# Kernel tuning notes

Hardware: AMD Instinct MI355X
Metric: run time of the kernel (lower is better)

## Reference

```python
import jax, jax.numpy as jnp
import numpy as np

B, S, D, H, F = 2, 2048, 1024, 16, 4096
HD = D // H
EPS = 1e-5
NEG = -1e9


def _layernorm(x, g, b):
    mu = jnp.mean(x, axis=-1, keepdims=True)
    var = jnp.mean((x - mu) ** 2, axis=-1, keepdims=True)
    return (x - mu) * jax.lax.rsqrt(var + EPS) * g + b


def _attention(x, wq, wk, wv, wo, bo):
    b, s, d = x.shape
    q = (x @ wq).reshape(b, s, H, HD).transpose(0, 2, 1, 3)  # [b,h,s,hd]
    k = (x @ wk).reshape(b, s, H, HD).transpose(0, 2, 1, 3)
    v = (x @ wv).reshape(b, s, H, HD).transpose(0, 2, 1, 3)
    scores = jnp.einsum('bhqd,bhkd->bhqk', q, k) / (HD ** 0.5)
    # Faithful to source bug: masked_fill(mask == 0, -1e9) where mask = triu(diag=1)
    # -> positions with k <= q (lower triangle incl. diagonal) are filled with -1e9.
    lower = jnp.tril(jnp.ones((s, s), dtype=bool))
    scores = jnp.where(lower, NEG, scores)
    w = jax.nn.softmax(scores, axis=-1)
    o = jnp.einsum('bhqk,bhkd->bhqd', w, v)
    o = o.transpose(0, 2, 1, 3).reshape(b, s, d)
    return o @ wo + bo


def _ffn(x, w1, b1, w2, b2):
    return jax.nn.gelu(x @ w1 + b1, approximate=False) @ w2 + b2


def setup_inputs() -> dict:
    key = jax.random.key(0)
    ks = jax.random.split(key, 10)
    s = 0.02
    return {
        'x': jax.random.normal(ks[0], (B, S, D), jnp.float32),
        'wq': jax.random.normal(ks[1], (D, D), jnp.float32) * s,
        'wk': jax.random.normal(ks[2], (D, D), jnp.float32) * s,
        'wv': jax.random.normal(ks[3], (D, D), jnp.float32) * s,
        'wo': jax.random.normal(ks[4], (D, D), jnp.float32) * s,
        'bo': jnp.zeros((D,), jnp.float32),
        'ln1_g': jnp.ones((D,), jnp.float32),
        'ln1_b': jnp.zeros((D,), jnp.float32),
        'ln2_g': jnp.ones((D,), jnp.float32),
        'ln2_b': jnp.zeros((D,), jnp.float32),
        'w1': jax.random.normal(ks[5], (D, F), jnp.float32) * s,
        'b1': jnp.zeros((F,), jnp.float32),
        'w2': jax.random.normal(ks[6], (F, D), jnp.float32) * s,
        'b2': jnp.zeros((D,), jnp.float32),
    }


def reference(x, wq, wk, wv, wo, bo, ln1_g, ln1_b, ln2_g, ln2_b, w1, b1, w2, b2):
    shortcut = x
    h = _layernorm(x, ln1_g, ln1_b)
    h = _attention(h, wq, wk, wv, wo, bo)  # dropout = identity (eval)
    h = h + shortcut
    shortcut = h
    h2 = _layernorm(h, ln2_g, ln2_b)
    h2 = _attention(h2, wq, wk, wv, wo, bo)  # same attn module reused, per source
    h2 = _ffn(h2, w1, b1, w2, b2)
    return h2 + shortcut
```

## Files before the change

kernel.cpp:

```cpp
#include <hip/hip_runtime.h>
#include <hip/hip_bf16.h>
#include <math.h>

#define Bz 2
#define Sz 2048
#define Dz 1024
#define Hz 16
#define HDz 64
#define Fz 4096
#define ROWS (Bz*Sz)
#define EPSf 1e-5f
#define NEGf -1e9f

typedef __attribute__((ext_vector_type(8))) short short8;
typedef __attribute__((ext_vector_type(4))) float floatx4;

__device__ __forceinline__ unsigned short f2bf(float f){
  __hip_bfloat16 h = __float2bfloat16(f);
  return *(unsigned short*)&h;
}
__device__ __forceinline__ float bf2f(unsigned short u){
  union { unsigned x; float f; } a; a.x = ((unsigned)u) << 16; return a.f;
}

__device__ __forceinline__ float fast_gelu(float x){
  float t  = fabsf(x) * 0.70710678118654752f;
  float kk = __builtin_amdgcn_rcpf(1.0f + 0.3275911f * t);
  float poly = ((((1.061405429f*kk - 1.453152027f)*kk + 1.421413741f)*kk
                 - 0.284496736f)*kk + 0.254829592f)*kk;
  float er = 1.0f - poly * __expf(-t*t);
  er = copysignf(er, x);
  return 0.5f * x * (1.0f + er);
}

__device__ __forceinline__ void gload16(const void* g, void* l){
  __builtin_amdgcn_global_load_lds(
      (const __attribute__((address_space(1))) unsigned int*)g,
      (__attribute__((address_space(3))) unsigned int*)l, 16, 0, 0);
}

__device__ __forceinline__ void bar(){
  asm volatile("" ::: "memory");
  __builtin_amdgcn_s_barrier();
  asm volatile("" ::: "memory");
}
#define WAITV6 asm volatile("s_waitcnt vmcnt(6)" ::: "memory")
#define WAITV0 asm volatile("s_waitcnt vmcnt(0)" ::: "memory")
#define WL0    asm volatile("s_waitcnt lgkmcnt(0)" ::: "memory")

__device__ __forceinline__ void xcd_remap(int& bmblk, int& bnblk){
  int gx = gridDim.x, gy = gridDim.y;
  int id = blockIdx.y * gx + blockIdx.x;
  int xcd = id & 7, local = id >> 3;
  bnblk = local % gx;
  bmblk = xcd * (gy >> 3) + local / gx;
}

__global__ __launch_bounds__(256)
void transpose_cast(const float* __restrict__ W, unsigned short* __restrict__ Wt,
                    int K, int N)
{
  __shared__ unsigned short Ts[32][33];
  int n0 = blockIdx.x*32, k0 = blockIdx.y*32;
  int r = threadIdx.x >> 3, c0 = (threadIdx.x & 7) * 4;
  float4 w4 = *(const float4*)(W + (size_t)(k0+r)*N + n0 + c0);
  Ts[r][c0+0] = f2bf(w4.x); Ts[r][c0+1] = f2bf(w4.y);
  Ts[r][c0+2] = f2bf(w4.z); Ts[r][c0+3] = f2bf(w4.w);
  __syncthreads();
  unsigned v0 = Ts[c0+0][r], v1 = Ts[c0+1][r], v2 = Ts[c0+2][r], v3 = Ts[c0+3][r];
  uint2 p; p.x = v0 | (v1<<16); p.y = v2 | (v3<<16);
  *(uint2*)(Wt + (size_t)(n0+r)*K + k0 + c0) = p;
}

__global__ __launch_bounds__(256)
void transpose_bf(const unsigned short* __restrict__ V, unsigned short* __restrict__ VT)
{
  __shared__ unsigned short Ts[32][33];
  int st = blockIdx.x*32;
  int R0 = blockIdx.y*32;
  int b = R0 >> 10, hd0 = R0 & 1023;
  int r = threadIdx.x >> 3, c0 = (threadIdx.x & 7) * 4;
  uint2 w = *(const uint2*)(V + (size_t)(b*Sz + st + r)*Dz + hd0 + c0);
  Ts[r][c0+0] = (unsigned short)(w.x & 0xffff);
  Ts[r][c0+1] = (unsigned short)(w.x >> 16);
  Ts[r][c0+2] = (unsigned short)(w.y & 0xffff);
  Ts[r][c0+3] = (unsigned short)(w.y >> 16);
  __syncthreads();
  unsigned v0 = Ts[c0+0][r], v1 = Ts[c0+1][r], v2 = Ts[c0+2][r], v3 = Ts[c0+3][r];
  uint2 p; p.x = v0 | (v1<<16); p.y = v2 | (v3<<16);
  *(uint2*)(VT + (size_t)(R0+r)*Sz + st + c0) = p;
}

__global__ __launch_bounds__(256)
void ln_kernel(const float* __restrict__ in, const float* __restrict__ gam,
               const float* __restrict__ bet, unsigned short* __restrict__ out)
{
  int row = blockIdx.x, t = threadIdx.x;
  size_t base = (size_t)row * Dz;
  int c0 = t * 4;
  float4 x4 = *(const float4*)(in + base + c0);
  float v[4] = {x4.x, x4.y, x4.z, x4.w};
  float s = v[0]+v[1]+v[2]+v[3];
  #pragma unroll
  for (int off=32; off>0; off>>=1) s += __shfl_down(s, off, 64);
  __shared__ float ws[4];
  int lane = t & 63, wid = t >> 6;
  if (lane == 0) ws[wid] = s;
  __syncthreads();
  float mu = (ws[0]+ws[1]+ws[2]+ws[3]) * (1.0f/Dz);
  __syncthreads();
  float d0=v[0]-mu, d1=v[1]-mu, d2=v[2]-mu, d3=v[3]-mu;
  float s2 = d0*d0+d1*d1+d2*d2+d3*d3;
  #pragma unroll
  for (int off=32; off>0; off>>=1) s2 += __shfl_down(s2, off, 64);
  if (lane == 0) ws[wid] = s2;
  __syncthreads();
  float var = (ws[0]+ws[1]+ws[2]+ws[3]) * (1.0f/Dz);
  float rstd = rsqrtf(var + EPSf);
  float4 g4 = *(const float4*)(gam + c0);
  float4 b4 = *(const float4*)(bet + c0);
  unsigned r0 = f2bf((v[0]-mu)*rstd*g4.x + b4.x);
  unsigned r1 = f2bf((v[1]-mu)*rstd*g4.y + b4.y);
  unsigned r2 = f2bf((v[2]-mu)*rstd*g4.z + b4.z);
  unsigned r3 = f2bf((v[3]-mu)*rstd*g4.w + b4.w);
  uint2 p; p.x = r0 | (r1<<16); p.y = r2 | (r3<<16);
  *(uint2*)(out + base + c0) = p;
}

#define STG_A(buf, half, k0) { \
  _Pragma("unroll") for (int c_=0;c_<2;c_++){ \
    int sg_ = c_*8 + wave; \
    int row0_ = ((sg_>>3)<<7) + ((sg_&7)<<3) + ((half)<<6); \
    gload16(pA[half][c_] + (k0), &As[buf][row0_*64]); } }

#define STG_B(buf, jh, k0) { \
  _Pragma("unroll") for (int c_=0;c_<2;c_++){ \
    int sg_ = c_*8 + wave; int rho0_ = sg_<<3; \
    gload16(pB[jh][c_] + (k0), &Bs[buf][jh][rho0_*64]); } }

#define READ_A4(dst, buf, ihalf) { \
  _Pragma("unroll") for (int ii_=0; ii_<4; ++ii_){ \
    int row_ = wm*128 + ((ihalf)*4+ii_)*16 + l15; \
    _Pragma("unroll") for (int ks_=0; ks_<2; ++ks_){ \
      int slot_ = (ks_*4+quad) ^ (l15&7); \
      dst[ii_][ks_] = *(const short8*)&As[buf][row_*64 + slot_*8]; } } }

#define READ_B2(dst, buf, jh) { \
  _Pragma("unroll") for (int jl_=0; jl_<2; ++jl_){ \
    int rho_ = wn*32 + jl_*16 + l15; \
    _Pragma("unroll") for (int ks_=0; ks_<2; ++ks_){ \
      int slot_ = (ks_*4+quad) ^ (l15&7); \
      dst[jl_][ks_] = *(const short8*)&Bs[buf][jh][rho_*64 + slot_*8]; } } }

#define MFMA_PH(IH, JH, AF, BF) { \
  __builtin_amdgcn_s_setprio(1); \
  _Pragma("unroll") for (int ii_=0; ii_<4; ++ii_){ \
    _Pragma("unroll") for (int jl_=0; jl_<2; ++jl_){ \
      floatx4 c_ = acc[(IH)*4+ii_][(JH)*2+jl_]; \
      c_ = __builtin_amdgcn_mfma_f32_16x16x32_bf16(AF[ii_][0], BF[jl_][0], c_, 0,0,0); \
      c_ = __builtin_amdgcn_mfma_f32_16x16x32_bf16(AF[ii_][1], BF[jl_][1], c_, 0,0,0); \
      acc[(IH)*4+ii_][(JH)*2+jl_] = c_; } } \
  __builtin_amdgcn_s_setprio(0); }

__global__ __launch_bounds__(512, 2)
void gemm256(const unsigned short* __restrict__ A,
             const unsigned short* __restrict__ Bt,
             const float* __restrict__ bias, const float* __restrict__ res,
             float* __restrict__ outf, unsigned short* __restrict__ outb,
             int M, int N, int K, int lda, int ldb, int act, int qkvmode)
{
  __shared__ unsigned short As[2][256*64];
  __shared__ unsigned short Bs[2][2][128*64];

  int t = threadIdx.x;
  int wave = t >> 6, lane = t & 63;
  int l15 = lane & 15, quad = lane >> 4;
  int wm = wave >> 2, wn = wave & 3;

  int nN = gridDim.x, nM = gridDim.y;
  int id = blockIdx.y * nN + blockIdx.x;
  int xcd = id & 7, local = id >> 3;
  int bnblk = local % nN;
  int bmblk = xcd * (nM >> 3) + local / nN;
  int bm = bmblk * 256, bn = bnblk * 256;

  if (gridDim.z > 1){
    A    += (size_t)blockIdx.z * K;
    Bt   += (size_t)blockIdx.z * K;
    outf += (size_t)blockIdx.z * ((size_t)M * N);
  }

  int lrow = lane >> 3;
  int lcol = ((lane & 7) ^ (lane >> 3)) * 8;

  const unsigned short* pA[2][2];
  const unsigned short* pB[2][2];
  #pragma unroll
  for (int half=0; half<2; half++)
    #pragma unroll
    for (int c=0;c<2;c++){
      int sg = c*8 + wave;
      int row0 = ((sg>>3)<<7) + ((sg&7)<<3) + (half<<6);
      pA[half][c] = A + (size_t)(bm + row0 + lrow)*lda + lcol;
    }
  #pragma unroll
  for (int jh=0; jh<2; jh++)
    #pragma unroll
    for (int c=0;c<2;c++){
      int sg = c*8 + wave;
      int rho0 = sg<<3;
      int gn = ((rho0>>5)<<6) + (jh<<5) + (rho0&31);
      pB[jh][c] = Bt + (size_t)(bn + gn + lrow)*ldb + lcol;
    }

  floatx4 acc[8][4];
  #pragma unroll
  for (int i=0;i<8;i++)
    #pragma unroll
    for (int j=0;j<4;j++) acc[i][j] = (floatx4){0.f,0.f,0.f,0.f};

  STG_A(0, 0, 0);  STG_A(0, 1, 0);
  STG_B(0, 0, 0);  STG_B(0, 1, 0);
  STG_A(1, 0, 64); STG_A(1, 1, 64);
  STG_B(1, 0, 64);
  WAITV6;
  bar();

  int NKT = K >> 6;
  int nIter = NKT >> 1;
  for (int it = 0; it < nIter; ++it){
    bool more = (it + 1 < nIter);
    int k0B  = (2*it+1) << 6;
    int k0A2 = (2*it+2) << 6;
    int k0B2 = (2*it+3) << 6;
    short8 aLo[4][2], aHi[4][2], bcur[2][2];

    READ_A4(aLo, 0, 0);
    READ_B2(bcur, 0, 0);
    STG_B(1, 1, k0B);
    bar(); WL0;
    MFMA_PH(0, 0, aLo, bcur);
    bar();

    READ_A4(aHi, 0, 1);
    READ_B2(bcur, 0, 0);
    if (more) STG_A(0, 0, k0A2);
    bar(); WL0;
    MFMA_PH(1, 0, aHi, bcur);
    bar();

    READ_B2(bcur, 0, 1);
    if (more) STG_A(0, 1, k0A2);
    bar(); WL0;
    MFMA_PH(0, 1, aLo, bcur);
    bar();

    if (more) { STG_B(0, 0, k0A2); WAITV6; }
    else      { WAITV0; }
    bar();
    MFMA_PH(1, 1, aHi, bcur);
    bar();

    READ_A4(aLo, 1, 0);
    READ_B2(bcur, 1, 0);
    if (more) STG_B(0, 1, k0A2);
    bar(); WL0;
    MFMA_PH(0, 0, aLo, bcur);
    bar();

    READ_A4(aHi, 1, 1);
    READ_B2(bcur, 1, 0);
    if (more) STG_A(1, 0, k0B2);
    bar(); WL0;
    MFMA_PH(1, 0, aHi, bcur);
    bar();

    READ_B2(bcur, 1, 1);
    if (more) STG_A(1, 1, k0B2);
    bar(); WL0;
    MFMA_PH(0, 1, aLo, bcur);
    bar();

    if (more) { STG_B(1, 0, k0B2); WAITV6; }
    bar();
    MFMA_PH(1, 1, aHi, bcur);
    bar();
  }

  float bj[4];
  #pragma unroll
  for (int j=0;j<4;j++) bj[j] = bias ? bias[bn + wn*64 + j*16 + l15] : 0.f;

  size_t selbase = 0; int ncol = N; int bnl = bn;
  if (qkvmode){ selbase = (size_t)(bn >> 10) * ((size_t)M * 1024); ncol = 1024; bnl = bn & 1023; }

  #pragma unroll
  for (int i=0;i<8;i++){
    int row0 = bm + wm*128 + i*16 + quad*4;
    #pragma unroll
    for (int r=0;r<4;r++){
      size_t rowoff = selbase + (size_t)(row0 + r) * ncol;
      #pragma unroll
      for (int j=0;j<4;j++){
        float v = acc[i][j][r] + bj[j];
        if (act) v = fast_gelu(v);
        size_t off = rowoff + bnl + wn*64 + j*16 + l15;
        if (res) v += res[off];
        if (outf) outf[off] = v;
        else      outb[off] = f2bf(v);
      }
    }
  }
}

__global__ __launch_bounds__(256)
void gemm_n64(const unsigned short* __restrict__ A,
              const unsigned short* __restrict__ Bt,
              const float* __restrict__ bias, const float* __restrict__ res,
              float* __restrict__ outf, unsigned short* __restrict__ outb,
              int M, int N, int K)
{
  __shared__ unsigned short As[2][128*64];
  __shared__ unsigned short Bs[2][64*64];
  int t = threadIdx.x;
  int bmblk, bnblk; xcd_remap(bmblk, bnblk);
  int bm = bmblk * 128, bn = bnblk * 64;
  int wave = t >> 6, lane = t & 63;
  int l15 = lane & 15, quad = lane >> 4;
  int arow = lane >> 3;
  int acbg = ((lane & 7) ^ arow) * 8;
  const unsigned short* gA = A  + (size_t)(bm + wave*32 + arow)*K + acbg;
  const unsigned short* gB = Bt + (size_t)(bn + wave*16 + arow)*K + acbg;

  floatx4 acc[2][4];
  #pragma unroll
  for (int i=0;i<2;i++)
    #pragma unroll
    for (int j=0;j<4;j++) acc[i][j] = (floatx4){0.f,0.f,0.f,0.f};

  int swr = (l15 & 7);

  {
    unsigned short* lA = &As[0][wave*32*64];
    unsigned short* lB = &Bs[0][wave*16*64];
    gload16(gA,                 lA);
    gload16(gA + (size_t)8*K,   lA + 8*64);
    gload16(gA + (size_t)16*K,  lA + 16*64);
    gload16(gA + (size_t)24*K,  lA + 24*64);
    gload16(gB,                 lB);
    gload16(gB + (size_t)8*K,   lB + 8*64);
  }

  int nIter = K >> 6;
  for (int it = 0; it < nIter; ++it) {
    __syncthreads();
    int cur = it & 1;
    if (it + 1 < nIter) {
      int k1 = (it+1) << 6;
      unsigned short* lA = &As[cur^1][wave*32*64];
      unsigned short* lB = &Bs[cur^1][wave*16*64];
      gload16(gA + k1,                 lA);
      gload16(gA + k1 + (size_t)8*K,   lA + 8*64);
      gload16(gA + k1 + (size_t)16*K,  lA + 16*64);
      gload16(gA + k1 + (size_t)24*K,  lA + 24*64);
      gload16(gB + k1,                 lB);
      gload16(gB + k1 + (size_t)8*K,   lB + 8*64);
    }
    const unsigned short* Ac = As[cur];
    const unsigned short* Bc = Bs[cur];
    #pragma unroll
    for (int ks=0; ks<2; ++ks){
      short8 af[2], bf[4];
      #pragma unroll
      for (int i=0;i<2;i++)
        af[i] = *(const short8*)&Ac[(wave*32 + i*16 + l15)*64 + ((ks*4 + quad) ^ swr)*8];
      #pragma unroll
      for (int j=0;j<4;j++)
        bf[j] = *(const short8*)&Bc[(j*16 + l15)*64 + ((ks*4 + quad) ^ swr)*8];
      #pragma unroll
      for (int i=0;i<2;i++)
        #pragma unroll
        for (int j=0;j<4;j++)
          acc[i][j] = __builtin_amdgcn_mfma_f32_16x16x32_bf16(af[i], bf[j], acc[i][j], 0, 0, 0);
    }
  }

  float bj[4];
  #pragma unroll
  for (int j=0;j<4;j++) bj[j] = bias ? bias[bn + j*16 + l15] : 0.f;

  #pragma unroll
  for (int i=0;i<2;i++){
    int row0 = bm + wave*32 + i*16 + quad*4;
    #pragma unroll
    for (int r=0;r<4;r++){
      size_t rowoff = (size_t)(row0 + r) * N;
      #pragma unroll
      for (int j=0;j<4;j++){
        float v = acc[i][j][r] + bj[j];
        size_t off = rowoff + bn + j*16 + l15;
        if (res) v += res[off];
        if (outf) outf[off] = v;
        else      outb[off] = f2bf(v);
      }
    }
  }
}

__global__ __launch_bounds__(256)
void reduce4(const float* __restrict__ part, const float* __restrict__ bias,
             const float* __restrict__ res, float* __restrict__ out)
{
  const size_t NN = (size_t)ROWS * Dz;
  size_t i = ((size_t)blockIdx.x * 256 + threadIdx.x) * 4;
  float4 a = *(const float4*)(part + i);
  float4 b = *(const float4*)(part + NN + i);
  float4 c = *(const float4*)(part + 2*NN + i);
  float4 d = *(const float4*)(part + 3*NN + i);
  float4 r = *(const float4*)(res + i);
  int col = threadIdx.x * 4;
  float4 g = *(const float4*)(bias + col);
  float4 o;
  o.x = a.x+b.x+c.x+d.x + g.x + r.x;
  o.y = a.y+b.y+c.y+d.y + g.y + r.y;
  o.z = a.z+b.z+c.z+d.z + g.z + r.z;
  o.w = a.w+b.w+c.w+d.w + g.w + r.w;
  *(float4*)(out + i) = o;
}

__global__ __launch_bounds__(256)
void vmean_kernel(const unsigned short* __restrict__ v, float* __restrict__ vm)
{
  int h = blockIdx.x, b = blockIdx.y;
  int t = threadIdx.x, d = t & 63, seg = t >> 6;
  float s = 0.f;
  for (int i=0;i<512;i++){
    int srow = seg*512 + i;
    s += bf2f(v[((size_t)(b*Sz + srow))*Dz + h*HDz + d]);
  }
  __shared__ float red[4][64];
  red[seg][d] = s;
  __syncthreads();
  if (seg == 0){
    float tot = red[0][d]+red[1][d]+red[2][d]+red[3][d];
    vm[(b*Hz + h)*HDz + d] = tot * (1.0f/2048.0f);
  }
}

__global__ __launch_bounds__(256)
void attn_mfma(const unsigned short* __restrict__ Qg,
               const unsigned short* __restrict__ Kg,
               const unsigned short* __restrict__ VTg,
               const float* __restrict__ vmean,
               unsigned short* __restrict__ Og)
{
  __shared__ unsigned short Ks[128*64];
  __shared__ unsigned short Vts[64*128];
  __shared__ unsigned short Ps[128][72];

  int t = threadIdx.x;
  int wave = t >> 6, lane = t & 63;
  int l15 = lane & 15, quad = lane >> 4;
  int b = blockIdx.z, h = blockIdx.y;
  int qt = b ? (15 - (int)blockIdx.x) : (int)blockIdx.x;

  {
    int r = t >> 1, c = (t & 1) * 32;
    const unsigned short* qp = Qg + ((size_t)(b*Sz + qt*128 + r))*Dz + h*HDz + c;
    uint4 q0 = *(const uint4*)(qp);
    uint4 q1 = *(const uint4*)(qp + 8);
    uint4 q2 = *(const uint4*)(qp + 16);
    uint4 q3 = *(const uint4*)(qp + 24);
    *(uint4*)&Ps[r][c]      = q0;
    *(uint4*)&Ps[r][c + 8]  = q1;
    *(uint4*)&Ps[r][c + 16] = q2;
    *(uint4*)&Ps[r][c + 24] = q3;
  }
  __syncthreads();
  short8 aq[2][2];
  #pragma unroll
  for (int i=0;i<2;i++)
    #pragma unroll
    for (int ks=0;ks<2;ks++)
      aq[i][ks] = *(const short8*)&Ps[wave*32 + i*16 + l15][ks*32 + quad*8];

  floatx4 acc_o[2][4];
  #pragma unroll
  for (int i=0;i<2;i++)
    #pragma unroll
    for (int j=0;j<4;j++) acc_o[i][j] = (floatx4){0.f,0.f,0.f,0.f};
  float lacc[2][4];
  #pragma unroll
  for (int i=0;i<2;i++)
    #pragma unroll
    for (int r=0;r<4;r++) lacc[i][r] = 0.f;

  int sr = t >> 2, sc = (t & 3) * 16;
  int kc2 = (t & 3) * 2, ksw = sr & 7;
  int vd = t >> 2, vc = t & 3, vsw = vd & 7;
  const unsigned short* vrow = VTg + ((size_t)((b*Hz + h)*64 + vd))*Sz;

  uint4 pk0,pk1,pk2,pk3,pv0,pv1,pv2,pv3;
  {
    size_t off0 = ((size_t)(b*Sz + qt*128 + sr))*Dz + h*HDz + sc;
    size_t off1 = off0 + (size_t)64*Dz;
    pk0 = *(const uint4*)(Kg + off0); pk1 = *(const uint4*)(Kg + off0 + 8);
    pk2 = *(const uint4*)(Kg + off1); pk3 = *(const uint4*)(Kg + off1 + 8);
    int vo = qt*128 + vc*32;
    pv0 = *(const uint4*)(vrow + vo);      pv1 = *(const uint4*)(vrow + vo + 8);
    pv2 = *(const uint4*)(vrow + vo + 16); pv3 = *(const uint4*)(vrow + vo + 24);
  }

  for (int jt2 = qt; jt2 < Sz/128; ++jt2) {
    __syncthreads();
    {
      *(uint4*)&Ks[sr*64      + ((kc2  ) ^ ksw)*8] = pk0;
      *(uint4*)&Ks[sr*64      + ((kc2+1) ^ ksw)*8] = pk1;
      *(uint4*)&Ks[(64+sr)*64 + ((kc2  ) ^ ksw)*8] = pk2;
      *(uint4*)&Ks[(64+sr)*64 + ((kc2+1) ^ ksw)*8] = pk3;
      int k80 = vc*4;
      *(uint4*)&Vts[vd*128 + (((k80+0)&8) | (((k80+0)^vsw)&7))*8] = pv0;
      *(uint4*)&Vts[vd*128 + (((k80+1)&8) | (((k80+1)^vsw)&7))*8] = pv1;
      *(uint4*)&Vts[vd*128 + (((k80+2)&8) | (((k80+2)^vsw)&7))*8] = pv2;
      *(uint4*)&Vts[vd*128 + (((k80+3)&8) | (((k80+3)^vsw)&7))*8] = pv3;
    }
    __syncthreads();

    if (jt2 + 1 < Sz/128) {
      size_t off0 = ((size_t)(b*Sz + (jt2+1)*128 + sr))*Dz + h*HDz + sc;
      size_t off1 = off0 + (size_t)64*Dz;
      pk0 = *(const uint4*)(Kg + off0); pk1 = *(const uint4*)(Kg + off0 + 8);
      pk2 = *(const uint4*)(Kg + off1); pk3 = *(const uint4*)(Kg + off1 + 8);
      int vo = (jt2+1)*128 + vc*32;
      pv0 = *(const uint4*)(vrow + vo);      pv1 = *(const uint4*)(vrow + vo + 8);
      pv2 = *(const uint4*)(vrow + vo + 16); pv3 = *(const uint4*)(vrow + vo + 24);
    }

    #pragma unroll
    for (int hh=0; hh<2; ++hh){
      floatx4 acc_s[2][4];
      #pragma unroll
      for (int i=0;i<2;i++)
        #pragma unroll
        for (int j=0;j<4;j++) acc_s[i][j] = (floatx4){0.f,0.f,0.f,0.f};
      #pragma unroll
      for (int ks=0;ks<2;ks++){
        short8 bk[4];
        #pragma unroll
        for (int j=0;j<4;j++)
          bk[j] = *(const short8*)&Ks[(hh*64 + j*16 + l15)*64 + (((ks*4+quad) ^ (l15&7)))*8];
        #pragma unroll
        for (int i=0;i<2;i++)
          #pragma unroll
          for (int j=0;j<4;j++)
            acc_s[i][j] = __builtin_amdgcn_mfma_f32_16x16x32_bf16(aq[i][ks], bk[j], acc_s[i][j], 0, 0, 0);
      }
      #pragma unroll
      for (int i=0;i<2;i++){
        #pragma unroll
        for (int j=0;j<4;j++){
          int kj = jt2*128 + hh*64 + j*16 + l15;
          #pragma unroll
          for (int r=0;r<4;r++){
            int qrow = qt*128 + wave*32 + i*16 + quad*4 + r;
            float s = acc_s[i][j][r] * 0.125f;
            if (kj <= qrow) s = NEGf;
            float p = __expf(fminf(s, 80.f));
            lacc[i][r] += p;
            Ps[wave*32 + i*16 + quad*4 + r][j*16 + l15] = f2bf(p);
          }
        }
      }
      #pragma unroll
      for (int ks=0;ks<2;ks++){
        short8 ap[2], bv[4];
        #pragma unroll
        for (int i=0;i<2;i++) ap[i] = *(const short8*)&Ps[wave*32 + i*16 + l15][ks*32 + quad*8];
        #pragma unroll
        for (int j=0;j<4;j++)
          bv[j] = *(const short8*)&Vts[(j*16 + l15)*128 + (hh*8 + ((ks*4+quad) ^ (l15&7)))*8];
        #pragma unroll
        for (int i=0;i<2;i++)
          #pragma unroll
          for (int j=0;j<4;j++)
            acc_o[i][j] = __builtin_amdgcn_mfma_f32_16x16x32_bf16(ap[i], bv[j], acc_o[i][j], 0, 0, 0);
      }
    }
  }

  #pragma unroll
  for (int i=0;i<2;i++){
    #pragma unroll
    for (int r=0;r<4;r++){
      float l = lacc[i][r];
      l += __shfl_xor(l, 1, 64);
      l += __shfl_xor(l, 2, 64);
      l += __shfl_xor(l, 4, 64);
      l += __shfl_xor(l, 8, 64);
      int qrow = qt*128 + wave*32 + i*16 + quad*4 + r;
      float inv = 1.0f / l;
      size_t rowoff = ((size_t)(b*Sz + qrow))*Dz + h*HDz;
      #pragma unroll
      for (int j=0;j<4;j++){
        float ov = acc_o[i][j][r] * inv;
        if (qrow == Sz-1) ov = vmean[(b*Hz + h)*HDz + j*16 + l15];
        Og[rowoff + j*16 + l15] = f2bf(ov);
      }
    }
  }
}

extern "C" void kernel_launch(void* const* d_in, const int* in_sizes, int n_in,
                              void* d_out, int out_size, void* d_ws, size_t ws_size,
                              hipStream_t stream)
{
  const float* x    = (const float*)d_in[0];
  const float* wq   = (const float*)d_in[1];
  const float* wk   = (const float*)d_in[2];
  const float* wv   = (const float*)d_in[3];
  const float* wo   = (const float*)d_in[4];
  const float* bo   = (const float*)d_in[5];
  const float* ln1g = (const float*)d_in[6];
  const float* ln1b = (const float*)d_in[7];
  const float* ln2g = (const float*)d_in[8];
  const float* ln2b = (const float*)d_in[9];
  const float* w1   = (const float*)d_in[10];
  const float* b1   = (const float*)d_in[11];
  const float* w2   = (const float*)d_in[12];
  const float* b2   = (const float*)d_in[13];
  float* out = (float*)d_out;

  const size_t MB = 1024*1024;
  char* w = (char*)d_ws;
  float*          trunk = (float*)(w);
  unsigned short* lnb   = (unsigned short*)(w + 16*MB);
  unsigned short* q     = (unsigned short*)(w + 24*MB);
  unsigned short* k     = (unsigned short*)(w + 32*MB);
  unsigned short* v     = (unsigned short*)(w + 40*MB);
  unsigned short* ctx   = (unsigned short*)(w + 48*MB);
  unsigned short* wqkvT = (unsigned short*)(w + 56*MB);
  unsigned short* wqT   = wqkvT;
  unsigned short* wkT   = (unsigned short*)(w + 58*MB);
  unsigned short* wvT   = (unsigned short*)(w + 60*MB);
  unsigned short* woT   = (unsigned short*)(w + 62*MB);
  unsigned short* w1T   = (unsigned short*)(w + 64*MB);
  unsigned short* w2T   = (unsigned short*)(w + 72*MB);
  unsigned short* mid   = (unsigned short*)(w + 24*MB);
  float*          part  = (float*)(w + 80*MB);
  bool splitk = ws_size >= (size_t)144*MB;

  unsigned short* vT    = (unsigned short*)d_out;
  float*          vmean = (float*)((char*)d_out + 8*MB);

  dim3 blk(256), blk512(512);
  transpose_cast<<<dim3(32,32),  blk, 0, stream>>>(wq, wqT, Dz, Dz);
  transpose_cast<<<dim3(32,32),  blk, 0, stream>>>(wk, wkT, Dz, Dz);
  transpose_cast<<<dim3(32,32),  blk, 0, stream>>>(wv, wvT, Dz, Dz);
  transpose_cast<<<dim3(32,32),  blk, 0, stream>>>(wo, woT, Dz, Dz);
  transpose_cast<<<dim3(128,32), blk, 0, stream>>>(w1, w1T, Dz, Fz);
  transpose_cast<<<dim3(32,128), blk, 0, stream>>>(w2, w2T, Fz, Dz);

  dim3 gln(ROWS);
  dim3 gqkv(3*Dz/256, ROWS/256);
  dim3 gf1(Fz/256,  ROWS/256);
  dim3 gn64(Dz/64,  ROWS/128);
  dim3 gattn(Sz/128, Hz, Bz);
  dim3 gvm(Hz, Bz);
  dim3 gvt(Sz/32, Bz*Hz*HDz/32);

  ln_kernel<<<gln, blk, 0, stream>>>(x, ln1g, ln1b, lnb);
  gemm256<<<gqkv, blk512, 0, stream>>>(lnb, wqkvT, nullptr, nullptr, nullptr, q, ROWS, 3*Dz, Dz, Dz, Dz, 0, 1);
  transpose_bf<<<gvt, blk, 0, stream>>>(v, vT);
  vmean_kernel<<<gvm, blk, 0, stream>>>(v, vmean);
  attn_mfma<<<gattn, blk, 0, stream>>>(q, k, vT, vmean, ctx);
  gemm_n64<<<gn64, blk, 0, stream>>>(ctx, woT, bo, x, trunk, nullptr, ROWS, Dz, Dz);

  ln_kernel<<<gln, blk, 0, stream>>>(trunk, ln2g, ln2b, lnb);
  gemm256<<<gqkv, blk512, 0, stream>>>(lnb, wqkvT, nullptr, nullptr, nullptr, q, ROWS, 3*Dz, Dz, Dz, Dz, 0, 1);
  transpose_bf<<<gvt, blk, 0, stream>>>(v, vT);
  vmean_kernel<<<gvm, blk, 0, stream>>>(v, vmean);
  attn_mfma<<<gattn, blk, 0, stream>>>(q, k, vT, vmean, ctx);
  gemm_n64<<<gn64, blk, 0, stream>>>(ctx, woT, bo, nullptr, nullptr, lnb, ROWS, Dz, Dz);
  gemm256<<<gf1, blk512, 0, stream>>>(lnb, w1T, b1, nullptr, nullptr, mid, ROWS, Fz, Dz, Dz, Dz, 1, 0);
  if (splitk) {
    gemm256<<<dim3(4,16,4), blk512, 0, stream>>>(mid, w2T, nullptr, nullptr, part, nullptr, ROWS, Dz, Fz/4, Fz, Fz, 0, 0);
    reduce4<<<dim3(4096), blk, 0, stream>>>(part, b2, trunk, out);
  } else {
    gemm_n64<<<gn64, blk, 0, stream>>>(mid, w2T, b2, trunk, out, nullptr, ROWS, Dz, Fz);
  }
}
```

Baseline: 537.5 us.

## Restructure attention kernel to 8 waves with 16 query rows each, peeled masked tile

The attention kernel moves from 256 to 512 threads per block, so each wave owns 16 query rows instead of 32, which halves per-wave accumulators and registers. The diagonal tile, the only one needing the causal mask, is peeled out so the remaining tiles skip mask checks. It also switches to exp2 with a folded scale and wraps MFMA phases in s_setprio hints. The aim is more waves in flight and less VALU work per tile, at the cost of more barrier participants and smaller per-thread load chunks.

```diff
diff --git a/kernel.cpp b/kernel.cpp
--- a/kernel.cpp
+++ b/kernel.cpp
@@ -11,6 +11,7 @@
 #define ROWS (Bz*Sz)
 #define EPSf 1e-5f
 #define NEGf -1e9f
+#define SC2f 0.1803368801111204f
 
 typedef __attribute__((ext_vector_type(8))) short short8;
 typedef __attribute__((ext_vector_type(4))) float floatx4;
@@ -447,7 +448,62 @@
   }
 }
 
-__global__ __launch_bounds__(256)
+#define ATT_STAGE_KV() { \
+    *(uint4*)&Ks[sr*64 + ((kc2  ) ^ ksw)*8] = pk0; \
+    *(uint4*)&Ks[sr*64 + ((kc2+1) ^ ksw)*8] = pk1; \
+    *(uint4*)&Vts[vd*128 + (((vk8  )&8) | (((vk8  )^vsw)&7))*8] = pv0; \
+    *(uint4*)&Vts[vd*128 + (((vk8+1)&8) | (((vk8+1)^vsw)&7))*8] = pv1; }
+
+#define ATT_PREFETCH(tile) { \
+    size_t off0_ = ((size_t)(b*Sz + (tile)*128 + sr))*Dz + h*HDz + sc; \
+    pk0 = *(const uint4*)(Kg + off0_); pk1 = *(const uint4*)(Kg + off0_ + 8); \
+    int vo_ = (tile)*128 + vc*16; \
+    pv0 = *(const uint4*)(vrow + vo_); pv1 = *(const uint4*)(vrow + vo_ + 8); }
+
+#define ATT_COMPUTE(MASKED) { \
+  _Pragma("unroll") \
+  for (int hh=0; hh<2; ++hh){ \
+    floatx4 acc_s[4]; \
+    _Pragma("unroll") for (int j=0;j<4;j++) acc_s[j] = (floatx4){0.f,0.f,0.f,0.f}; \
+    __builtin_amdgcn_s_setprio(1); \
+    _Pragma("unroll") \
+    for (int ks=0;ks<2;ks++){ \
+      short8 bk[4]; \
+      _Pragma("unroll") \
+      for (int j=0;j<4;j++) \
+        bk[j] = *(const short8*)&Ks[(hh*64 + j*16 + l15)*64 + (((ks*4+quad) ^ (l15&7)))*8]; \
+      _Pragma("unroll") \
+      for (int j=0;j<4;j++) \
+        acc_s[j] = __builtin_amdgcn_mfma_f32_16x16x32_bf16(aq[ks], bk[j], acc_s[j], 0, 0, 0); \
+    } \
+    __builtin_amdgcn_s_setprio(0); \
+    _Pragma("unroll") \
+    for (int j=0;j<4;j++){ \
+      _Pragma("unroll") \
+      for (int r=0;r<4;r++){ \
+        float s2 = acc_s[j][r] * SC2f; \
+        if (MASKED){ int kloc = hh*64 + j*16 + l15; if (kloc <= qloc + r) s2 = NEGf; } \
+        float p = __builtin_amdgcn_exp2f(fminf(s2, 115.41f)); \
+        lacc[r] += p; \
+        Ps[wave*16 + quad*4 + r][j*16 + l15] = f2bf(p); \
+      } \
+    } \
+    __builtin_amdgcn_s_setprio(1); \
+    _Pragma("unroll") \
+    for (int ks=0;ks<2;ks++){ \
+      short8 ap, bv[4]; \
+      ap = *(const short8*)&Ps[wave*16 + l15][ks*32 + quad*8]; \
+      _Pragma("unroll") \
+      for (int j=0;j<4;j++) \
+        bv[j] = *(const short8*)&Vts[(j*16 + l15)*128 + (hh*8 + ((ks*4+quad) ^ (l15&7)))*8]; \
+      _Pragma("unroll") \
+      for (int j=0;j<4;j++) \
+        acc_o[j] = __builtin_amdgcn_mfma_f32_16x16x32_bf16(ap, bv[j], acc_o[j], 0, 0, 0); \
+    } \
+    __builtin_amdgcn_s_setprio(0); \
+  } }
+
+__global__ __launch_bounds__(512, 4)
 void attn_mfma(const unsigned short* __restrict__ Qg,
                const unsigned short* __restrict__ Kg,
                const unsigned short* __restrict__ VTg,
@@ -465,147 +521,63 @@
   int qt = b ? (15 - (int)blockIdx.x) : (int)blockIdx.x;
 
   {
-    int r = t >> 1, c = (t & 1) * 32;
+    int r = t >> 2, c = (t & 3) * 16;
     const unsigned short* qp = Qg + ((size_t)(b*Sz + qt*128 + r))*Dz + h*HDz + c;
     uint4 q0 = *(const uint4*)(qp);
     uint4 q1 = *(const uint4*)(qp + 8);
-    uint4 q2 = *(const uint4*)(qp + 16);
-    uint4 q3 = *(const uint4*)(qp + 24);
-    *(uint4*)&Ps[r][c]      = q0;
-    *(uint4*)&Ps[r][c + 8]  = q1;
-    *(uint4*)&Ps[r][c + 16] = q2;
-    *(uint4*)&Ps[r][c + 24] = q3;
-  }
-  __syncthreads();
-  short8 aq[2][2];
-  #pragma unroll
-  for (int i=0;i<2;i++)
-    #pragma unroll
-    for (int ks=0;ks<2;ks++)
-      aq[i][ks] = *(const short8*)&Ps[wave*32 + i*16 + l15][ks*32 + quad*8];
-
-  floatx4 acc_o[2][4];
-  #pragma unroll
-  for (int i=0;i<2;i++)
-    #pragma unroll
-    for (int j=0;j<4;j++) acc_o[i][j] = (floatx4){0.f,0.f,0.f,0.f};
-  float lacc[2][4];
-  #pragma unroll
-  for (int i=0;i<2;i++)
-    #pragma unroll
-    for (int r=0;r<4;r++) lacc[i][r] = 0.f;
+    *(uint4*)&Ps[r][c]     = q0;
+    *(uint4*)&Ps[r][c + 8] = q1;
+  }
 
   int sr = t >> 2, sc = (t & 3) * 16;
   int kc2 = (t & 3) * 2, ksw = sr & 7;
-  int vd = t >> 2, vc = t & 3, vsw = vd & 7;
+  int vd = t >> 3, vc = t & 7, vsw = vd & 7;
+  int vk8 = vc * 2;
   const unsigned short* vrow = VTg + ((size_t)((b*Hz + h)*64 + vd))*Sz;
 
-  uint4 pk0,pk1,pk2,pk3,pv0,pv1,pv2,pv3;
-  {
-    size_t off0 = ((size_t)(b*Sz + qt*128 + sr))*Dz + h*HDz + sc;
-    size_t off1 = off0 + (size_t)64*Dz;
-    pk0 = *(const uint4*)(Kg + off0); pk1 = *(const uint4*)(Kg + off0 + 8);
-    pk2 = *(const uint4*)(Kg + off1); pk3 = *(const uint4*)(Kg + off1 + 8);
-    int vo = qt*128 + vc*32;
-    pv0 = *(const uint4*)(vrow + vo);      pv1 = *(const uint4*)(vrow + vo + 8);
-    pv2 = *(const uint4*)(vrow + vo + 16); pv3 = *(const uint4*)(vrow + vo + 24);
-  }
-
-  for (int jt2 = qt; jt2 < Sz/128; ++jt2) {
+  uint4 pk0, pk1, pv0, pv1;
+  ATT_PREFETCH(qt);
+
+  __syncthreads();
+  short8 aq[2];
+  aq[0] = *(const short8*)&Ps[wave*16 + l15][quad*8];
+  aq[1] = *(const short8*)&Ps[wave*16 + l15][32 + quad*8];
+
+  floatx4 acc_o[4];
+  #pragma unroll
+  for (int j=0;j<4;j++) acc_o[j] = (floatx4){0.f,0.f,0.f,0.f};
+  float lacc[4] = {0.f, 0.f, 0.f, 0.f};
+
+  int qloc = wave*16 + quad*4;
+
+  ATT_STAGE_KV();
+  __syncthreads();
+  if (qt + 1 < Sz/128) ATT_PREFETCH(qt+1);
+  ATT_COMPUTE(1);
+
+  for (int jt2 = qt+1; jt2 < Sz/128; ++jt2){
     __syncthreads();
-    {
-      *(uint4*)&Ks[sr*64      + ((kc2  ) ^ ksw)*8] = pk0;
-      *(uint4*)&Ks[sr*64      + ((kc2+1) ^ ksw)*8] = pk1;
-      *(uint4*)&Ks[(64+sr)*64 + ((kc2  ) ^ ksw)*8] = pk2;
-      *(uint4*)&Ks[(64+sr)*64 + ((kc2+1) ^ ksw)*8] = pk3;
-      int k80 = vc*4;
-      *(uint4*)&Vts[vd*128 + (((k80+0)&8) | (((k80+0)^vsw)&7))*8] = pv0;
-      *(uint4*)&Vts[vd*128 + (((k80+1)&8) | (((k80+1)^vsw)&7))*8] = pv1;
-      *(uint4*)&Vts[vd*128 + (((k80+2)&8) | (((k80+2)^vsw)&7))*8] = pv2;
-      *(uint4*)&Vts[vd*128 + (((k80+3)&8) | (((k80+3)^vsw)&7))*8] = pv3;
-    }
+    ATT_STAGE_KV();
     __syncthreads();
-
-    if (jt2 + 1 < Sz/128) {
-      size_t off0 = ((size_t)(b*Sz + (jt2+1)*128 + sr))*Dz + h*HDz + sc;
-      size_t off1 = off0 + (size_t)64*Dz;
-      pk0 = *(const uint4*)(Kg + off0); pk1 = *(const uint4*)(Kg + off0 + 8);
-      pk2 = *(const uint4*)(Kg + off1); pk3 = *(const uint4*)(Kg + off1 + 8);
-      int vo = (jt2+1)*128 + vc*32;
-      pv0 = *(const uint4*)(vrow + vo);      pv1 = *(const uint4*)(vrow + vo + 8);
-      pv2 = *(const uint4*)(vrow + vo + 16); pv3 = *(const uint4*)(vrow + vo + 24);
-    }
-
-    #pragma unroll
-    for (int hh=0; hh<2; ++hh){
-      floatx4 acc_s[2][4];
-      #pragma unroll
-      for (int i=0;i<2;i++)
-        #pragma unroll
-        for (int j=0;j<4;j++) acc_s[i][j] = (floatx4){0.f,0.f,0.f,0.f};
-      #pragma unroll
-      for (int ks=0;ks<2;ks++){
-        short8 bk[4];
-        #pragma unroll
-        for (int j=0;j<4;j++)
-          bk[j] = *(const short8*)&Ks[(hh*64 + j*16 + l15)*64 + (((ks*4+quad) ^ (l15&7)))*8];
-        #pragma unroll
-        for (int i=0;i<2;i++)
-          #pragma unroll
-          for (int j=0;j<4;j++)
-            acc_s[i][j] = __builtin_amdgcn_mfma_f32_16x16x32_bf16(aq[i][ks], bk[j], acc_s[i][j], 0, 0, 0);
-      }
-      #pragma unroll
-      for (int i=0;i<2;i++){
-        #pragma unroll
-        for (int j=0;j<4;j++){
-          int kj = jt2*128 + hh*64 + j*16 + l15;
-          #pragma unroll
-          for (int r=0;r<4;r++){
-            int qrow = qt*128 + wave*32 + i*16 + quad*4 + r;
-            float s = acc_s[i][j][r] * 0.125f;
-            if (kj <= qrow) s = NEGf;
-            float p = __expf(fminf(s, 80.f));
-            lacc[i][r] += p;
-            Ps[wave*32 + i*16 + quad*4 + r][j*16 + l15] = f2bf(p);
-          }
-        }
-      }
-      #pragma unroll
-      for (int ks=0;ks<2;ks++){
-        short8 ap[2], bv[4];
-        #pragma unroll
-        for (int i=0;i<2;i++) ap[i] = *(const short8*)&Ps[wave*32 + i*16 + l15][ks*32 + quad*8];
-        #pragma unroll
-        for (int j=0;j<4;j++)
-          bv[j] = *(const short8*)&Vts[(j*16 + l15)*128 + (hh*8 + ((ks*4+quad) ^ (l15&7)))*8];
-        #pragma unroll
-        for (int i=0;i<2;i++)
-          #pragma unroll
-          for (int j=0;j<4;j++)
-            acc_o[i][j] = __builtin_amdgcn_mfma_f32_16x16x32_bf16(ap[i], bv[j], acc_o[i][j], 0, 0, 0);
-      }
-    }
-  }
-
-  #pragma unroll
-  for (int i=0;i<2;i++){
-    #pragma unroll
-    for (int r=0;r<4;r++){
-      float l = lacc[i][r];
-      l += __shfl_xor(l, 1, 64);
-      l += __shfl_xor(l, 2, 64);
-      l += __shfl_xor(l, 4, 64);
-      l += __shfl_xor(l, 8, 64);
-      int qrow = qt*128 + wave*32 + i*16 + quad*4 + r;
-      float inv = 1.0f / l;
-      size_t rowoff = ((size_t)(b*Sz + qrow))*Dz + h*HDz;
-      #pragma unroll
-      for (int j=0;j<4;j++){
-        float ov = acc_o[i][j][r] * inv;
-        if (qrow == Sz-1) ov = vmean[(b*Hz + h)*HDz + j*16 + l15];
-        Og[rowoff + j*16 + l15] = f2bf(ov);
-      }
+    if (jt2 + 1 < Sz/128) ATT_PREFETCH(jt2+1);
+    ATT_COMPUTE(0);
+  }
+
+  #pragma unroll
+  for (int r=0;r<4;r++){
+    float l = lacc[r];
+    l += __shfl_xor(l, 1, 64);
+    l += __shfl_xor(l, 2, 64);
+    l += __shfl_xor(l, 4, 64);
+    l += __shfl_xor(l, 8, 64);
+    int qrow = qt*128 + wave*16 + quad*4 + r;
+    float inv = 1.0f / l;
+    size_t rowoff = ((size_t)(b*Sz + qrow))*Dz + h*HDz;
+    #pragma unroll
+    for (int j=0;j<4;j++){
+      float ov = acc_o[j][r] * inv;
+      if (qrow == Sz-1) ov = vmean[(b*Hz + h)*HDz + j*16 + l15];
+      Og[rowoff + j*16 + l15] = f2bf(ov);
     }
   }
 }
@@ -672,14 +644,14 @@
   gemm256<<<gqkv, blk512, 0, stream>>>(lnb, wqkvT, nullptr, nullptr, nullptr, q, ROWS, 3*Dz, Dz, Dz, Dz, 0, 1);
   transpose_bf<<<gvt, blk, 0, stream>>>(v, vT);
   vmean_kernel<<<gvm, blk, 0, stream>>>(v, vmean);
-  attn_mfma<<<gattn, blk, 0, stream>>>(q, k, vT, vmean, ctx);
+  attn_mfma<<<gattn, blk512, 0, stream>>>(q, k, vT, vmean, ctx);
   gemm_n64<<<gn64, blk, 0, stream>>>(ctx, woT, bo, x, trunk, nullptr, ROWS, Dz, Dz);
 
   ln_kernel<<<gln, blk, 0, stream>>>(trunk, ln2g, ln2b, lnb);
   gemm256<<<gqkv, blk512, 0, stream>>>(lnb, wqkvT, nullptr, nullptr, nullptr, q, ROWS, 3*Dz, Dz, Dz, Dz, 0, 1);
   transpose_bf<<<gvt, blk, 0, stream>>>(v, vT);
   vmean_kernel<<<gvm, blk, 0, stream>>>(v, vmean);
-  attn_mfma<<<gattn, blk, 0, stream>>>(q, k, vT, vmean, ctx);
+  attn_mfma<<<gattn, blk512, 0, stream>>>(q, k, vT, vmean, ctx);
   gemm_n64<<<gn64, blk, 0, stream>>>(ctx, woT, bo, nullptr, nullptr, lnb, ROWS, Dz, Dz);
   gemm256<<<gf1, blk512, 0, stream>>>(lnb, w1T, b1, nullptr, nullptr, mid, ROWS, Fz, Dz, Dz, Dz, 1, 0);
   if (splitk) {
```

Result: faster. 510.8 us (-5.0%).
